# Performance work log

Hardware: AMD Instinct MI355X
Metric: run time of the kernel (lower is better)

Reference implementation:

```python
import jax, jax.numpy as jnp
from jax import lax
import numpy as np

H_DIM = 256
BETA = 0.1
BATCH = 32768
N_STEPS = 32
DT = 0.01
GAIN_TANH = 5.0 / 3.0  # nn.init.calculate_gain('tanh')


def _xavier_uniform(key, fan_out, fan_in, gain):
    limit = gain * jnp.sqrt(6.0 / (fan_in + fan_out))
    return jax.random.uniform(key, (fan_out, fan_in), dtype=jnp.float32,
                              minval=-limit, maxval=limit)


def setup_inputs() -> dict:
    key = jax.random.key(0)
    ks = jax.random.split(key, 6)
    t_eval = jnp.arange(N_STEPS, dtype=jnp.float32) * DT
    state0 = 0.1 * jax.random.normal(ks[0], (BATCH, 4), dtype=jnp.float32)
    W1 = _xavier_uniform(ks[1], H_DIM, 4, GAIN_TANH)
    W2 = _xavier_uniform(ks[2], H_DIM, H_DIM, GAIN_TANH)
    W3 = _xavier_uniform(ks[3], H_DIM, H_DIM, GAIN_TANH)
    W4 = _xavier_uniform(ks[4], 1, H_DIM, GAIN_TANH)
    b1 = jnp.zeros((H_DIM,), jnp.float32)
    b2 = jnp.zeros((H_DIM,), jnp.float32)
    b3 = jnp.zeros((H_DIM,), jnp.float32)
    b4 = jnp.zeros((1,), jnp.float32)
    scale = jnp.asarray(0.005, dtype=jnp.float32)
    return {"t_eval": t_eval, "state0": state0,
            "W1": W1, "b1": b1, "W2": W2, "b2": b2,
            "W3": W3, "b3": b3, "W4": W4, "b4": b4, "scale": scale}


def _hamiltonian_sum(s, W1, b1, W2, b2, W3, b3, W4, b4):
    # 4 -> h -> h -> h -> 1 tanh MLP; sum over batch so grad gives per-sample dH/ds
    h = jnp.tanh(s @ W1.T + b1)
    h = jnp.tanh(h @ W2.T + b2)
    h = jnp.tanh(h @ W3.T + b3)
    return jnp.sum(h @ W4.T + b4)


def _verlet_step(state, dt):
    # exact Henon-Heiles velocity-verlet; state: (B, 4) = (q1, p1, q2, p2)
    q1, p1, q2, p2 = state[:, 0], state[:, 1], state[:, 2], state[:, 3]
    F1 = -q1 * (1.0 + 2.0 * q2)
    F2 = -(q2 + q1 ** 2 - q2 ** 2)
    p1h = p1 + 0.5 * dt * F1
    p2h = p2 + 0.5 * dt * F2
    q1n = q1 + dt * p1h
    q2n = q2 + dt * p2h
    F1n = -q1n * (1.0 + 2.0 * q2n)
    F2n = -(q2n + q1n ** 2 - q2n ** 2)
    p1n = p1h + 0.5 * dt * F1n
    p2n = p2h + 0.5 * dt * F2n
    return jnp.stack([q1n, p1n, q2n, p2n], axis=1)


def reference(t_eval, state0, W1, b1, W2, b2, W3, b3, W4, b4, scale):
    dt = t_eval[1] - t_eval[0]
    n_steps = t_eval.shape[0]

    def corr_dyn(state):
        # torch detaches the state before the autograd-Hamiltonian gradient
        s = lax.stop_gradient(state)
        g = jax.grad(_hamiltonian_sum)(s, W1, b1, W2, b2, W3, b3, W4, b4)  # (B,4)
        # symplectic rotation of grad_H: (dq1, dp1, dq2, dp2)
        return jnp.stack([g[:, 1], -g[:, 0], g[:, 3], -g[:, 2]], axis=1)

    def step(state, _):
        corr = corr_dyn(state)
        corr_norm = jnp.linalg.norm(corr, axis=1, keepdims=True)  # (B,1)
        adapt_dt = lax.stop_gradient(
            dt * jnp.clip(1.0 - BETA * corr_norm, 0.5, 1.0))
        new_state = _verlet_step(state, dt) + adapt_dt * (scale * corr)
        return new_state, new_state

    _, traj = lax.scan(step, state0, None, length=n_steps - 1)  # (T-1, B, 4)
    full = jnp.concatenate([state0[None], traj], axis=0)        # (T, B, 4)
    return jnp.transpose(full, (1, 0, 2))                        # (B, T, 4)
```

## Files before the change

### kernel.cpp

```cpp
#include <hip/hip_runtime.h>
#include <hip/hip_bf16.h>
#include <math.h>

#define H       256
#define TB      64
#define NT      1024
#define NSTEPS  32
#define XS      264
#define DS1     260

typedef __attribute__((ext_vector_type(8))) short short8v;
typedef __attribute__((ext_vector_type(4))) float f32x4;

__device__ __forceinline__ float fast_tanh(float x) {
    float e;
    asm("v_exp_f32 %0, %1" : "=v"(e) : "v"(x * 2.8853900817779268f));
    return fmaf(-2.0f, __builtin_amdgcn_rcpf(e + 1.0f), 1.0f);
}

__device__ __forceinline__ unsigned pk2(float lo, float hi) {
    __hip_bfloat162 h2 = __float22bfloat162_rn(make_float2(lo, hi));
    unsigned u; __builtin_memcpy(&u, &h2, 4);
    return u;
}
__device__ __forceinline__ unsigned short f2b(float x) {
    unsigned u = __float_as_uint(x);
    u += 0x7FFFu + ((u >> 16) & 1u);
    return (unsigned short)(u >> 16);
}
__device__ __forceinline__ float b2f(unsigned short h) {
    return __uint_as_float(((unsigned)h) << 16);
}

__global__ void convert_w(const float* __restrict__ W2, const float* __restrict__ W3,
                          unsigned short* __restrict__ wsb) {
    int t = blockIdx.x * blockDim.x + threadIdx.x;
    int i = t >> 8, j = t & 255;
    float w2 = W2[t], w3 = W3[t];
    wsb[t]                         = f2b(w2);
    wsb[65536 + t]                 = f2b(w3);
    wsb[131072 + (j << 8) + i]     = f2b(w2);
    wsb[196608 + (j << 8) + i]     = f2b(w3);
}

#define GLW(dst, base, OFFB)                                                   \
    asm volatile("global_load_dwordx4 %0, %1, off offset:" #OFFB               \
                 : "=v"(dst) : "v"(base));
#define LOADW(w, base)                                                         \
    GLW(w[0], base, 0)   GLW(w[1], base, 64)  GLW(w[2], base, 128)             \
    GLW(w[3], base, 192) GLW(w[4], base, 256) GLW(w[5], base, 320)             \
    GLW(w[6], base, 384) GLW(w[7], base, 448)                                  \
    asm volatile("s_waitcnt vmcnt(0)" ::: "memory");                           \
    __builtin_amdgcn_sched_barrier(0);

#define MFMA_CHAIN(WREG, XSRC)                                                 \
    _Pragma("unroll")                                                          \
    for (int kc = 0; kc < 8; ++kc) {                                           \
        short8v b0 = *reinterpret_cast<const short8v*>(&XSRC[sl][kc*32 + kg*8]);      \
        short8v b1 = *reinterpret_cast<const short8v*>(&XSRC[16 + sl][kc*32 + kg*8]); \
        short8v b2v = *reinterpret_cast<const short8v*>(&XSRC[32 + sl][kc*32 + kg*8]);\
        short8v b3v = *reinterpret_cast<const short8v*>(&XSRC[48 + sl][kc*32 + kg*8]);\
        acc0 = __builtin_amdgcn_mfma_f32_16x16x32_bf16(WREG[kc], b0,  acc0, 0, 0, 0); \
        acc1 = __builtin_amdgcn_mfma_f32_16x16x32_bf16(WREG[kc], b1,  acc1, 0, 0, 0); \
        acc2 = __builtin_amdgcn_mfma_f32_16x16x32_bf16(WREG[kc], b2v, acc2, 0, 0, 0); \
        acc3 = __builtin_amdgcn_mfma_f32_16x16x32_bf16(WREG[kc], b3v, acc3, 0, 0, 0); \
    }

__global__ __launch_bounds__(NT)
void sympnet_mfma(const float* __restrict__ t_eval,
                  const float* __restrict__ state0,
                  const float* __restrict__ W1, const float* __restrict__ b1,
                  const float* __restrict__ b2, const float* __restrict__ b3,
                  const float* __restrict__ W4, const float* __restrict__ scale_p,
                  const short* __restrict__ W2b,  const short* __restrict__ W3b,
                  const short* __restrict__ W2Tb, const short* __restrict__ W3Tb,
                  float* __restrict__ out)
{
    __shared__ unsigned short Xa[TB][XS];
    __shared__ unsigned short Xb[TB][XS];
    __shared__ unsigned short D1[TB][DS1];
    __shared__ float sS[TB][4];
    __shared__ float gp[16][TB][4];
    __shared__ float sW1[H * 4];
    __shared__ float sB1[H], sB2[H], sB3[H], sW4[H];

    const int tid  = threadIdx.x;
    const int lane = tid & 63;
    const int wv   = tid >> 6;
    const int sl   = lane & 15;
    const int kg   = lane >> 4;
    const int n0   = wv * 16;

    const float dt    = t_eval[1] - t_eval[0];
    const float scale = scale_p[0];
    const int   b0    = blockIdx.x * TB;

    const short* W2p  = W2b  + ((n0 + sl) << 8) + kg * 8;
    const short* W3p  = W3b  + ((n0 + sl) << 8) + kg * 8;
    const short* W3Tp = W3Tb + ((n0 + sl) << 8) + kg * 8;
    const short* W2Tp = W2Tb + ((n0 + sl) << 8) + kg * 8;

    if (tid < H) {
        reinterpret_cast<float4*>(sW1)[tid] = reinterpret_cast<const float4*>(W1)[tid];
        sB1[tid] = b1[tid];
        sB2[tid] = b2[tid];
        sB3[tid] = b3[tid];
        sW4[tid] = W4[tid];
    }
    if (tid < TB) {
        float4 s = reinterpret_cast<const float4*>(state0)[b0 + tid];
        sS[tid][0] = s.x; sS[tid][1] = s.y; sS[tid][2] = s.z; sS[tid][3] = s.w;
        reinterpret_cast<float4*>(out)[(size_t)(b0 + tid) * NSTEPS] = s;
    }
    __syncthreads();

    unsigned d2p[8];

    for (int t = 1; t < NSTEPS; ++t) {
        {
            const int j0 = (tid & 31) * 8;
            const int r0 = (tid >> 5) * 2;
            float4 wvv[8];
            #pragma unroll
            for (int jj = 0; jj < 8; ++jj)
                wvv[jj] = reinterpret_cast<const float4*>(sW1)[j0 + jj];
            float bb[8];
            #pragma unroll
            for (int jj = 0; jj < 8; ++jj) bb[jj] = sB1[j0 + jj];
            #pragma unroll
            for (int ii = 0; ii < 2; ++ii) {
                float4 sv = *reinterpret_cast<const float4*>(&sS[r0 + ii][0]);
                float h[8], d[8];
                #pragma unroll
                for (int jj = 0; jj < 8; ++jj) {
                    float z = bb[jj] + sv.x * wvv[jj].x + sv.y * wvv[jj].y
                                     + sv.z * wvv[jj].z + sv.w * wvv[jj].w;
                    h[jj] = fast_tanh(z);
                    d[jj] = fmaf(-h[jj], h[jj], 1.0f);
                }
                *reinterpret_cast<uint2*>(&Xa[r0 + ii][j0]) =
                    make_uint2(pk2(h[0], h[1]), pk2(h[2], h[3]));
                *reinterpret_cast<uint2*>(&Xa[r0 + ii][j0 + 4]) =
                    make_uint2(pk2(h[4], h[5]), pk2(h[6], h[7]));
                *reinterpret_cast<uint2*>(&D1[r0 + ii][j0]) =
                    make_uint2(pk2(d[0], d[1]), pk2(d[2], d[3]));
                *reinterpret_cast<uint2*>(&D1[r0 + ii][j0 + 4]) =
                    make_uint2(pk2(d[4], d[5]), pk2(d[6], d[7]));
            }
        }
        __syncthreads();

        {
            short8v w[8];
            LOADW(w, W2p);
            f32x4 acc0 = {}, acc1 = {}, acc2 = {}, acc3 = {};
            MFMA_CHAIN(w, Xa);
            float4 bv = *reinterpret_cast<const float4*>(&sB2[n0 + kg * 4]);
            const float* bp = reinterpret_cast<const float*>(&bv);
            #pragma unroll
            for (int mt = 0; mt < 4; ++mt) {
                f32x4 acc = (mt == 0) ? acc0 : (mt == 1) ? acc1 : (mt == 2) ? acc2 : acc3;
                float h[4], d[4];
                #pragma unroll
                for (int rr = 0; rr < 4; ++rr) {
                    h[rr] = fast_tanh(acc[rr] + bp[rr]);
                    d[rr] = fmaf(-h[rr], h[rr], 1.0f);
                }
                d2p[mt*2]     = pk2(d[0], d[1]);
                d2p[mt*2 + 1] = pk2(d[2], d[3]);
                *reinterpret_cast<uint2*>(&Xb[mt*16 + sl][n0 + kg*4]) =
                    make_uint2(pk2(h[0], h[1]), pk2(h[2], h[3]));
            }
        }
        __syncthreads();

        {
            short8v w[8];
            LOADW(w, W3p);
            f32x4 acc0 = {}, acc1 = {}, acc2 = {}, acc3 = {};
            MFMA_CHAIN(w, Xb);
            float4 bv  = *reinterpret_cast<const float4*>(&sB3[n0 + kg * 4]);
            float4 wv4 = *reinterpret_cast<const float4*>(&sW4[n0 + kg * 4]);
            const float* bp = reinterpret_cast<const float*>(&bv);
            const float* wp = reinterpret_cast<const float*>(&wv4);
            #pragma unroll
            for (int mt = 0; mt < 4; ++mt) {
                f32x4 acc = (mt == 0) ? acc0 : (mt == 1) ? acc1 : (mt == 2) ? acc2 : acc3;
                float u[4];
                #pragma unroll
                for (int rr = 0; rr < 4; ++rr) {
                    float h = fast_tanh(acc[rr] + bp[rr]);
                    u[rr] = wp[rr] * fmaf(-h, h, 1.0f);
                }
                *reinterpret_cast<uint2*>(&Xa[mt*16 + sl][n0 + kg*4]) =
                    make_uint2(pk2(u[0], u[1]), pk2(u[2], u[3]));
            }
        }
        __syncthreads();

        {
            short8v w[8];
            LOADW(w, W3Tp);
            f32x4 acc0 = {}, acc1 = {}, acc2 = {}, acc3 = {};
            MFMA_CHAIN(w, Xa);
            #pragma unroll
            for (int mt = 0; mt < 4; ++mt) {
                f32x4 acc = (mt == 0) ? acc0 : (mt == 1) ? acc1 : (mt == 2) ? acc2 : acc3;
                float dd[4] = { b2f((unsigned short)(d2p[mt*2]   & 0xffffu)),
                                b2f((unsigned short)(d2p[mt*2]   >> 16)),
                                b2f((unsigned short)(d2p[mt*2+1] & 0xffffu)),
                                b2f((unsigned short)(d2p[mt*2+1] >> 16)) };
                float u[4];
                #pragma unroll
                for (int rr = 0; rr < 4; ++rr)
                    u[rr] = acc[rr] * dd[rr];
                *reinterpret_cast<uint2*>(&Xb[mt*16 + sl][n0 + kg*4]) =
                    make_uint2(pk2(u[0], u[1]), pk2(u[2], u[3]));
            }
        }
        __syncthreads();

        {
            short8v w[8];
            LOADW(w, W2Tp);
            f32x4 acc0 = {}, acc1 = {}, acc2 = {}, acc3 = {};
            MFMA_CHAIN(w, Xb);
            float4 w1v[4];
            #pragma unroll
            for (int rr = 0; rr < 4; ++rr)
                w1v[rr] = reinterpret_cast<const float4*>(sW1)[n0 + kg*4 + rr];
            #pragma unroll
            for (int mt = 0; mt < 4; ++mt) {
                f32x4 acc = (mt == 0) ? acc0 : (mt == 1) ? acc1 : (mt == 2) ? acc2 : acc3;
                short4 dv = *reinterpret_cast<const short4*>(&D1[mt*16 + sl][n0 + kg*4]);
                float dd[4] = { b2f((unsigned short)dv.x), b2f((unsigned short)dv.y),
                                b2f((unsigned short)dv.z), b2f((unsigned short)dv.w) };
                float pg0 = 0.f, pg1 = 0.f, pg2 = 0.f, pg3 = 0.f;
                #pragma unroll
                for (int rr = 0; rr < 4; ++rr) {
                    float u1 = acc[rr] * dd[rr];
                    float4 w = w1v[rr];
                    pg0 = fmaf(u1, w.x, pg0); pg1 = fmaf(u1, w.y, pg1);
                    pg2 = fmaf(u1, w.z, pg2); pg3 = fmaf(u1, w.w, pg3);
                }
                pg0 += __shfl_xor(pg0, 16); pg1 += __shfl_xor(pg1, 16);
                pg2 += __shfl_xor(pg2, 16); pg3 += __shfl_xor(pg3, 16);
                pg0 += __shfl_xor(pg0, 32); pg1 += __shfl_xor(pg1, 32);
                pg2 += __shfl_xor(pg2, 32); pg3 += __shfl_xor(pg3, 32);
                if (kg == 0)
                    *reinterpret_cast<float4*>(&gp[wv][mt*16 + sl][0]) =
                        make_float4(pg0, pg1, pg2, pg3);
            }
        }
        __syncthreads();

        if (tid < TB) {
            float g0 = 0.f, g1 = 0.f, g2 = 0.f, g3 = 0.f;
            #pragma unroll
            for (int w = 0; w < 16; ++w) {
                float4 p = *reinterpret_cast<const float4*>(&gp[w][tid][0]);
                g0 += p.x; g1 += p.y; g2 += p.z; g3 += p.w;
            }
            float c0 = g1, c1 = -g0, c2 = g3, c3 = -g2;
            float nrm = sqrtf(c0*c0 + c1*c1 + c2*c2 + c3*c3);
            float ad  = dt * fminf(fmaxf(1.0f - 0.1f * nrm, 0.5f), 1.0f);
            float q1  = sS[tid][0], p1v = sS[tid][1];
            float q2  = sS[tid][2], p2v = sS[tid][3];
            float F1  = -q1 * (1.0f + 2.0f * q2);
            float F2  = -(q2 + q1 * q1 - q2 * q2);
            float p1h = p1v + 0.5f * dt * F1;
            float p2h = p2v + 0.5f * dt * F2;
            float q1n = q1 + dt * p1h;
            float q2n = q2 + dt * p2h;
            float F1n = -q1n * (1.0f + 2.0f * q2n);
            float F2n = -(q2n + q1n * q1n - q2n * q2n);
            float p1n = p1h + 0.5f * dt * F1n;
            float p2n = p2h + 0.5f * dt * F2n;
            float as  = ad * scale;
            float ns0 = q1n + as * c0;
            float ns1 = p1n + as * c1;
            float ns2 = q2n + as * c2;
            float ns3 = p2n + as * c3;
            sS[tid][0] = ns0; sS[tid][1] = ns1; sS[tid][2] = ns2; sS[tid][3] = ns3;
            reinterpret_cast<float4*>(out)[(size_t)(b0 + tid) * NSTEPS + t] =
                make_float4(ns0, ns1, ns2, ns3);
        }
        __syncthreads();
    }
}

extern "C" void kernel_launch(void* const* d_in, const int* in_sizes, int n_in,
                              void* d_out, int out_size, void* d_ws, size_t ws_size,
                              hipStream_t stream) {
    const float* t_eval = (const float*)d_in[0];
    const float* state0 = (const float*)d_in[1];
    const float* W1     = (const float*)d_in[2];
    const float* b1     = (const float*)d_in[3];
    const float* W2     = (const float*)d_in[4];
    const float* b2     = (const float*)d_in[5];
    const float* W3     = (const float*)d_in[6];
    const float* b3     = (const float*)d_in[7];
    const float* W4     = (const float*)d_in[8];
    const float* scale  = (const float*)d_in[10];
    float* out = (float*)d_out;

    unsigned short* wsb = (unsigned short*)d_ws;
    convert_w<<<dim3(256), dim3(256), 0, stream>>>(W2, W3, wsb);

    const short* W2b  = (const short*)(wsb);
    const short* W3b  = (const short*)(wsb + 65536);
    const short* W2Tb = (const short*)(wsb + 131072);
    const short* W3Tb = (const short*)(wsb + 196608);

    const int batch = in_sizes[1] / 4;
    sympnet_mfma<<<dim3(batch / TB), dim3(NT), 0, stream>>>(
        t_eval, state0, W1, b1, b2, b3, W4, scale,
        W2b, W3b, W2Tb, W3Tb, out);
}
```

Baseline: 1.503 ms.

## Retile MFMA work so each wave computes 2x2 output/sample tiles

Each of the 16 waves previously computed a 16-output slice across all 64 samples, loading 8 weight fragments and reading all 64 sample rows from LDS. Waves now split into 8 output groups of 32 and 2 sample groups of 32, so each wave loads two weight fragments and reads only half the activations, reusing each LDS B-fragment across two weight tiles. This halves LDS activation reads per wave but doubles the per-wave weight register footprint and global weight loads, and the gradient partial buffer shrinks to 8 slices.

```diff
diff --git a/kernel.cpp b/kernel.cpp
--- a/kernel.cpp
+++ b/kernel.cpp
@@ -46,25 +46,27 @@
 #define GLW(dst, base, OFFB)                                                   \
     asm volatile("global_load_dwordx4 %0, %1, off offset:" #OFFB               \
                  : "=v"(dst) : "v"(base));
-#define LOADW(w, base)                                                         \
-    GLW(w[0], base, 0)   GLW(w[1], base, 64)  GLW(w[2], base, 128)             \
-    GLW(w[3], base, 192) GLW(w[4], base, 256) GLW(w[5], base, 320)             \
-    GLW(w[6], base, 384) GLW(w[7], base, 448)                                  \
+#define LOADW2(w0, p0, w1, p1)                                                 \
+    GLW(w0[0], p0, 0)   GLW(w0[1], p0, 64)  GLW(w0[2], p0, 128)                \
+    GLW(w0[3], p0, 192) GLW(w0[4], p0, 256) GLW(w0[5], p0, 320)                \
+    GLW(w0[6], p0, 384) GLW(w0[7], p0, 448)                                    \
+    GLW(w1[0], p1, 0)   GLW(w1[1], p1, 64)  GLW(w1[2], p1, 128)                \
+    GLW(w1[3], p1, 192) GLW(w1[4], p1, 256) GLW(w1[5], p1, 320)                \
+    GLW(w1[6], p1, 384) GLW(w1[7], p1, 448)                                    \
     asm volatile("s_waitcnt vmcnt(0)" ::: "memory");                           \
     __builtin_amdgcn_sched_barrier(0);
 
-#define MFMA_CHAIN(WREG, XSRC)                                                 \
+#define MFMA_CHAIN(W0, W1, XSRC)                                               \
     _Pragma("unroll")                                                          \
     for (int kc = 0; kc < 8; ++kc) {                                           \
-        short8v b0 = *reinterpret_cast<const short8v*>(&XSRC[sl][kc*32 + kg*8]);      \
-        short8v b1 = *reinterpret_cast<const short8v*>(&XSRC[16 + sl][kc*32 + kg*8]); \
-        short8v b2v = *reinterpret_cast<const short8v*>(&XSRC[32 + sl][kc*32 + kg*8]);\
-        short8v b3v = *reinterpret_cast<const short8v*>(&XSRC[48 + sl][kc*32 + kg*8]);\
-        acc0 = __builtin_amdgcn_mfma_f32_16x16x32_bf16(WREG[kc], b0,  acc0, 0, 0, 0); \
-        acc1 = __builtin_amdgcn_mfma_f32_16x16x32_bf16(WREG[kc], b1,  acc1, 0, 0, 0); \
-        acc2 = __builtin_amdgcn_mfma_f32_16x16x32_bf16(WREG[kc], b2v, acc2, 0, 0, 0); \
-        acc3 = __builtin_amdgcn_mfma_f32_16x16x32_bf16(WREG[kc], b3v, acc3, 0, 0, 0); \
+        short8v bb0 = *reinterpret_cast<const short8v*>(&XSRC[ms][kc*32 + kg*8]);      \
+        short8v bb1 = *reinterpret_cast<const short8v*>(&XSRC[ms + 16][kc*32 + kg*8]); \
+        a00 = __builtin_amdgcn_mfma_f32_16x16x32_bf16(W0[kc], bb0, a00, 0, 0, 0);      \
+        a01 = __builtin_amdgcn_mfma_f32_16x16x32_bf16(W0[kc], bb1, a01, 0, 0, 0);      \
+        a10 = __builtin_amdgcn_mfma_f32_16x16x32_bf16(W1[kc], bb0, a10, 0, 0, 0);      \
+        a11 = __builtin_amdgcn_mfma_f32_16x16x32_bf16(W1[kc], bb1, a11, 0, 0, 0);      \
     }
+#define ACC_SEL(ot, st) ((ot) == 0 ? ((st) == 0 ? a00 : a01) : ((st) == 0 ? a10 : a11))
 
 __global__ __launch_bounds__(NT)
 void sympnet_mfma(const float* __restrict__ t_eval,
@@ -80,16 +82,19 @@
     __shared__ unsigned short Xb[TB][XS];
     __shared__ unsigned short D1[TB][DS1];
     __shared__ float sS[TB][4];
-    __shared__ float gp[16][TB][4];
+    __shared__ float gp[8][TB][4];
     __shared__ float sW1[H * 4];
     __shared__ float sB1[H], sB2[H], sB3[H], sW4[H];
 
     const int tid  = threadIdx.x;
     const int lane = tid & 63;
     const int wv   = tid >> 6;
+    const int og   = wv & 7;
+    const int sg   = wv >> 3;
     const int sl   = lane & 15;
     const int kg   = lane >> 4;
-    const int n0   = wv * 16;
+    const int n0   = og * 32;
+    const int ms   = sg * 32 + sl;
 
     const float dt    = t_eval[1] - t_eval[0];
     const float scale = scale_p[0];
@@ -151,105 +156,129 @@
         __syncthreads();
 
         {
-            short8v w[8];
-            LOADW(w, W2p);
-            f32x4 acc0 = {}, acc1 = {}, acc2 = {}, acc3 = {};
-            MFMA_CHAIN(w, Xa);
-            float4 bv = *reinterpret_cast<const float4*>(&sB2[n0 + kg * 4]);
-            const float* bp = reinterpret_cast<const float*>(&bv);
-            #pragma unroll
-            for (int mt = 0; mt < 4; ++mt) {
-                f32x4 acc = (mt == 0) ? acc0 : (mt == 1) ? acc1 : (mt == 2) ? acc2 : acc3;
-                float h[4], d[4];
-                #pragma unroll
-                for (int rr = 0; rr < 4; ++rr) {
-                    h[rr] = fast_tanh(acc[rr] + bp[rr]);
-                    d[rr] = fmaf(-h[rr], h[rr], 1.0f);
-                }
-                d2p[mt*2]     = pk2(d[0], d[1]);
-                d2p[mt*2 + 1] = pk2(d[2], d[3]);
-                *reinterpret_cast<uint2*>(&Xb[mt*16 + sl][n0 + kg*4]) =
-                    make_uint2(pk2(h[0], h[1]), pk2(h[2], h[3]));
-            }
-        }
-        __syncthreads();
-
-        {
-            short8v w[8];
-            LOADW(w, W3p);
-            f32x4 acc0 = {}, acc1 = {}, acc2 = {}, acc3 = {};
-            MFMA_CHAIN(w, Xb);
-            float4 bv  = *reinterpret_cast<const float4*>(&sB3[n0 + kg * 4]);
-            float4 wv4 = *reinterpret_cast<const float4*>(&sW4[n0 + kg * 4]);
-            const float* bp = reinterpret_cast<const float*>(&bv);
-            const float* wp = reinterpret_cast<const float*>(&wv4);
-            #pragma unroll
-            for (int mt = 0; mt < 4; ++mt) {
-                f32x4 acc = (mt == 0) ? acc0 : (mt == 1) ? acc1 : (mt == 2) ? acc2 : acc3;
-                float u[4];
-                #pragma unroll
-                for (int rr = 0; rr < 4; ++rr) {
-                    float h = fast_tanh(acc[rr] + bp[rr]);
-                    u[rr] = wp[rr] * fmaf(-h, h, 1.0f);
-                }
-                *reinterpret_cast<uint2*>(&Xa[mt*16 + sl][n0 + kg*4]) =
-                    make_uint2(pk2(u[0], u[1]), pk2(u[2], u[3]));
-            }
-        }
-        __syncthreads();
-
-        {
-            short8v w[8];
-            LOADW(w, W3Tp);
-            f32x4 acc0 = {}, acc1 = {}, acc2 = {}, acc3 = {};
-            MFMA_CHAIN(w, Xa);
-            #pragma unroll
-            for (int mt = 0; mt < 4; ++mt) {
-                f32x4 acc = (mt == 0) ? acc0 : (mt == 1) ? acc1 : (mt == 2) ? acc2 : acc3;
-                float dd[4] = { b2f((unsigned short)(d2p[mt*2]   & 0xffffu)),
-                                b2f((unsigned short)(d2p[mt*2]   >> 16)),
-                                b2f((unsigned short)(d2p[mt*2+1] & 0xffffu)),
-                                b2f((unsigned short)(d2p[mt*2+1] >> 16)) };
-                float u[4];
+            short8v w0[8], w1[8];
+            const short* p1 = W2p + 4096;
+            LOADW2(w0, W2p, w1, p1);
+            f32x4 a00 = {}, a01 = {}, a10 = {}, a11 = {};
+            MFMA_CHAIN(w0, w1, Xa);
+            #pragma unroll
+            for (int ot = 0; ot < 2; ++ot) {
+                float4 bv = *reinterpret_cast<const float4*>(&sB2[n0 + ot*16 + kg*4]);
+                const float* bp = reinterpret_cast<const float*>(&bv);
+                #pragma unroll
+                for (int st = 0; st < 2; ++st) {
+                    f32x4 acc = ACC_SEL(ot, st);
+                    float h[4], d[4];
+                    #pragma unroll
+                    for (int rr = 0; rr < 4; ++rr) {
+                        h[rr] = fast_tanh(acc[rr] + bp[rr]);
+                        d[rr] = fmaf(-h[rr], h[rr], 1.0f);
+                    }
+                    d2p[(ot*2 + st)*2]     = pk2(d[0], d[1]);
+                    d2p[(ot*2 + st)*2 + 1] = pk2(d[2], d[3]);
+                    *reinterpret_cast<uint2*>(&Xb[sg*32 + st*16 + sl][n0 + ot*16 + kg*4]) =
+                        make_uint2(pk2(h[0], h[1]), pk2(h[2], h[3]));
+                }
+            }
+        }
+        __syncthreads();
+
+        {
+            short8v w0[8], w1[8];
+            const short* p1 = W3p + 4096;
+            LOADW2(w0, W3p, w1, p1);
+            f32x4 a00 = {}, a01 = {}, a10 = {}, a11 = {};
+            MFMA_CHAIN(w0, w1, Xb);
+            #pragma unroll
+            for (int ot = 0; ot < 2; ++ot) {
+                float4 bv  = *reinterpret_cast<const float4*>(&sB3[n0 + ot*16 + kg*4]);
+                float4 wv4 = *reinterpret_cast<const float4*>(&sW4[n0 + ot*16 + kg*4]);
+                const float* bp = reinterpret_cast<const float*>(&bv);
+                const float* wp = reinterpret_cast<const float*>(&wv4);
+                #pragma unroll
+                for (int st = 0; st < 2; ++st) {
+                    f32x4 acc = ACC_SEL(ot, st);
+                    float u[4];
+                    #pragma unroll
+                    for (int rr = 0; rr < 4; ++rr) {
+                        float h = fast_tanh(acc[rr] + bp[rr]);
+                        u[rr] = wp[rr] * fmaf(-h, h, 1.0f);
+                    }
+                    *reinterpret_cast<uint2*>(&Xa[sg*32 + st*16 + sl][n0 + ot*16 + kg*4]) =
+                        make_uint2(pk2(u[0], u[1]), pk2(u[2], u[3]));
+                }
+            }
+        }
+        __syncthreads();
+
+        {
+            short8v w0[8], w1[8];
+            const short* p1 = W3Tp + 4096;
+            LOADW2(w0, W3Tp, w1, p1);
+            f32x4 a00 = {}, a01 = {}, a10 = {}, a11 = {};
+            MFMA_CHAIN(w0, w1, Xa);
+            #pragma unroll
+            for (int ot = 0; ot < 2; ++ot) {
+                #pragma unroll
+                for (int st = 0; st < 2; ++st) {
+                    f32x4 acc = ACC_SEL(ot, st);
+                    const int di = (ot*2 + st)*2;
+                    float dd[4] = { b2f((unsigned short)(d2p[di]   & 0xffffu)),
+                                    b2f((unsigned short)(d2p[di]   >> 16)),
+                                    b2f((unsigned short)(d2p[di+1] & 0xffffu)),
+                                    b2f((unsigned short)(d2p[di+1] >> 16)) };
+                    float u[4];
+                    #pragma unroll
+                    for (int rr = 0; rr < 4; ++rr)
+                        u[rr] = acc[rr] * dd[rr];
+                    *reinterpret_cast<uint2*>(&Xb[sg*32 + st*16 + sl][n0 + ot*16 + kg*4]) =
+                        make_uint2(pk2(u[0], u[1]), pk2(u[2], u[3]));
+                }
+            }
+        }
+        __syncthreads();
+
+        {
+            short8v w0[8], w1[8];
+            const short* p1 = W2Tp + 4096;
+            LOADW2(w0, W2Tp, w1, p1);
+            f32x4 a00 = {}, a01 = {}, a10 = {}, a11 = {};
+            MFMA_CHAIN(w0, w1, Xb);
+            float pg[2][4] = {};
+            #pragma unroll
+            for (int ot = 0; ot < 2; ++ot) {
+                float4 w1v[4];
                 #pragma unroll
                 for (int rr = 0; rr < 4; ++rr)
-                    u[rr] = acc[rr] * dd[rr];
-                *reinterpret_cast<uint2*>(&Xb[mt*16 + sl][n0 + kg*4]) =
-                    make_uint2(pk2(u[0], u[1]), pk2(u[2], u[3]));
-            }
-        }
-        __syncthreads();
-
-        {
-            short8v w[8];
-            LOADW(w, W2Tp);
-            f32x4 acc0 = {}, acc1 = {}, acc2 = {}, acc3 = {};
-            MFMA_CHAIN(w, Xb);
-            float4 w1v[4];
-            #pragma unroll
-            for (int rr = 0; rr < 4; ++rr)
-                w1v[rr] = reinterpret_cast<const float4*>(sW1)[n0 + kg*4 + rr];
-            #pragma unroll
-            for (int mt = 0; mt < 4; ++mt) {
-                f32x4 acc = (mt == 0) ? acc0 : (mt == 1) ? acc1 : (mt == 2) ? acc2 : acc3;
-                short4 dv = *reinterpret_cast<const short4*>(&D1[mt*16 + sl][n0 + kg*4]);
-                float dd[4] = { b2f((unsigned short)dv.x), b2f((unsigned short)dv.y),
-                                b2f((unsigned short)dv.z), b2f((unsigned short)dv.w) };
-                float pg0 = 0.f, pg1 = 0.f, pg2 = 0.f, pg3 = 0.f;
-                #pragma unroll
-                for (int rr = 0; rr < 4; ++rr) {
-                    float u1 = acc[rr] * dd[rr];
-                    float4 w = w1v[rr];
-                    pg0 = fmaf(u1, w.x, pg0); pg1 = fmaf(u1, w.y, pg1);
-                    pg2 = fmaf(u1, w.z, pg2); pg3 = fmaf(u1, w.w, pg3);
-                }
-                pg0 += __shfl_xor(pg0, 16); pg1 += __shfl_xor(pg1, 16);
-                pg2 += __shfl_xor(pg2, 16); pg3 += __shfl_xor(pg3, 16);
-                pg0 += __shfl_xor(pg0, 32); pg1 += __shfl_xor(pg1, 32);
-                pg2 += __shfl_xor(pg2, 32); pg3 += __shfl_xor(pg3, 32);
+                    w1v[rr] = reinterpret_cast<const float4*>(sW1)[n0 + ot*16 + kg*4 + rr];
+                #pragma unroll
+                for (int st = 0; st < 2; ++st) {
+                    f32x4 acc = ACC_SEL(ot, st);
+                    short4 dv = *reinterpret_cast<const short4*>(
+                        &D1[sg*32 + st*16 + sl][n0 + ot*16 + kg*4]);
+                    float dd[4] = { b2f((unsigned short)dv.x), b2f((unsigned short)dv.y),
+                                    b2f((unsigned short)dv.z), b2f((unsigned short)dv.w) };
+                    #pragma unroll
+                    for (int rr = 0; rr < 4; ++rr) {
+                        float u1 = acc[rr] * dd[rr];
+                        float4 w = w1v[rr];
+                        pg[st][0] = fmaf(u1, w.x, pg[st][0]);
+                        pg[st][1] = fmaf(u1, w.y, pg[st][1]);
+                        pg[st][2] = fmaf(u1, w.z, pg[st][2]);
+                        pg[st][3] = fmaf(u1, w.w, pg[st][3]);
+                    }
+                }
+            }
+            #pragma unroll
+            for (int st = 0; st < 2; ++st) {
+                float p0 = pg[st][0], p1v = pg[st][1], p2 = pg[st][2], p3 = pg[st][3];
+                p0 += __shfl_xor(p0, 16); p1v += __shfl_xor(p1v, 16);
+                p2 += __shfl_xor(p2, 16); p3 += __shfl_xor(p3, 16);
+                p0 += __shfl_xor(p0, 32); p1v += __shfl_xor(p1v, 32);
+                p2 += __shfl_xor(p2, 32); p3 += __shfl_xor(p3, 32);
                 if (kg == 0)
-                    *reinterpret_cast<float4*>(&gp[wv][mt*16 + sl][0]) =
-                        make_float4(pg0, pg1, pg2, pg3);
+                    *reinterpret_cast<float4*>(&gp[og][sg*32 + st*16 + sl][0]) =
+                        make_float4(p0, p1v, p2, p3);
             }
         }
         __syncthreads();
@@ -257,7 +286,7 @@
         if (tid < TB) {
             float g0 = 0.f, g1 = 0.f, g2 = 0.f, g3 = 0.f;
             #pragma unroll
-            for (int w = 0; w < 16; ++w) {
+            for (int w = 0; w < 8; ++w) {
                 float4 p = *reinterpret_cast<const float4*>(&gp[w][tid][0]);
                 g0 += p.x; g1 += p.y; g2 += p.z; g3 += p.w;
             }
```

New measurement: 2.329 ms. 54.9% more time.
